# Optimization experiments

Hardware: AMD Instinct MI355X
Metric: run time of the kernel (lower is better)

Reference implementation:

```python
import jax, jax.numpy as jnp
import numpy as np

BETA = 0.1
IGNORE_INDEX = -100
B, T, H, V = 4, 512, 2048, 32000


def setup_inputs() -> dict:
    key = jax.random.key(0)
    k1, k2, k3, k4, k5 = jax.random.split(key, 5)
    x = jax.random.normal(k1, (B, T, H), dtype=jnp.float32)
    ref_x = jax.random.normal(k2, (B, T, H), dtype=jnp.float32)
    y = jax.random.randint(k3, (B, T), 0, V, dtype=jnp.int64)
    W = jax.random.normal(k4, (V, H), dtype=jnp.float32) * 0.02
    ref_W = jax.random.normal(k5, (V, H), dtype=jnp.float32) * 0.02
    return {"x": x, "ref_x": ref_x, "y": y, "W": W, "ref_W": ref_W}


def _avg_logps(inp, weight, target):
    # inp: [B,T,H], weight: [V,H], target: [B,T]
    logits = jnp.einsum('bth,vh->btv', inp, weight)          # [B,T,V]
    lse = jax.nn.logsumexp(logits, axis=-1)                  # [B,T]
    mask = (target != IGNORE_INDEX)
    safe = jnp.where(mask, target, 0)
    tok = jnp.take_along_axis(logits, safe[..., None], axis=-1)[..., 0]
    per_token_logps = tok - lse                               # [B,T]
    mask_f = mask.astype(per_token_logps.dtype)
    return (per_token_logps * mask_f).sum(-1) / mask_f.sum(-1)  # [B]


def reference(x, ref_x, y, W, ref_W):
    half = y.shape[0] // 2
    policy_logps = _avg_logps(x, W, y)
    # reference model runs under no_grad in the original
    ref_logps = jax.lax.stop_gradient(_avg_logps(ref_x, ref_W, y))
    logratios = policy_logps - ref_logps                      # [B]
    kl = jnp.zeros((), dtype=logratios.dtype)                 # kl=None -> 0
    chosen_losses = 1.0 - jax.nn.sigmoid(BETA * (logratios[:half] - kl))
    rejected_losses = 1.0 - jax.nn.sigmoid(BETA * (kl - logratios[half:]))
    return (chosen_losses.sum() + rejected_losses.sum()) / half
```

## Files before the change

kernel.cpp:

```cpp
#include <hip/hip_runtime.h>
#include <stdint.h>

#define B_DIM 4
#define T_DIM 512
#define NTOK  2048
#define H_DIM 2048
#define V_DIM 32000
#define BETA   0.1f
#define IGNORE_INDEX (-100)

#define TM    128
#define TN    128
#define BK    64
#define NCHUNK 250
#define NCH8  125
#define NTILE8 8

typedef _Float16 f16;
typedef _Float16 half8 __attribute__((ext_vector_type(8)));
typedef float    f32x4 __attribute__((ext_vector_type(4)));

#define AS1(p) ((const __attribute__((address_space(1))) unsigned int*)(p))
#define AS3(p) ((__attribute__((address_space(3))) unsigned int*)(p))

__global__ __launch_bounds__(256) void cvt_f32_f16(const float* __restrict__ src,
                                                   f16* __restrict__ dst, int n) {
    int i = (blockIdx.x * 256 + threadIdx.x) * 8;
    if (i + 8 > n) return;
    float4 v0 = *(const float4*)(src + i);
    float4 v1 = *(const float4*)(src + i + 4);
    half8 h = { (f16)v0.x, (f16)v0.y, (f16)v0.z, (f16)v0.w,
                (f16)v1.x, (f16)v1.y, (f16)v1.z, (f16)v1.w };
    *(half8*)(dst + i) = h;
}


#define DSR(d, a, IMM) \
    asm volatile("ds_read_b128 %0, %1 offset:%2" : "=v"(d) : "v"(a), "n"(IMM))

#define KTSTEP(BUF, KTW) do {                                                  \
    half8 af[4];                                                               \
    DSR(af[0], A_rd, (BUF) * 32768 + 0);                                       \
    DSR(af[1], A_rd, (BUF) * 32768 + 256);                                     \
    DSR(af[2], A_rd, (BUF) * 32768 + 512);                                     \
    DSR(af[3], A_rd, (BUF) * 32768 + 768);                                     \
    DSR(bfp[0], B_rd, (BUF) * 32768 + 0);                                      \
    DSR(bfp[1], B_rd, (BUF) * 32768 + 256);                                    \
    DSR(bfp[2], B_rd, (BUF) * 32768 + 512);                                    \
    DSR(bfp[3], B_rd, (BUF) * 32768 + 768);                                    \
    {                                                                          \
        const f16* sA = pA + (KTW) * 32;                                       \
        const f16* sB = pB + (KTW) * 32;                                       \
        f16* tA = dA + ((BUF) ^ 1) * 16384;                                    \
        f16* tB = dB + ((BUF) ^ 1) * 16384;                                    \
        __builtin_amdgcn_global_load_lds(AS1(sA),      AS3(tA),        16, 0, 0); \
        __builtin_amdgcn_global_load_lds(AS1(sA + 16), AS3(tA + 4096), 16, 0, 0); \
        __builtin_amdgcn_global_load_lds(AS1(sB),      AS3(tB),        16, 0, 0); \
        __builtin_amdgcn_global_load_lds(AS1(sB + 16), AS3(tB + 4096), 16, 0, 0); \
    }                                                                          \
    __builtin_amdgcn_s_barrier();                                              \
    asm volatile("s_waitcnt lgkmcnt(0)" ::: "memory");                         \
    __builtin_amdgcn_sched_barrier(0);                                         \
    __builtin_amdgcn_s_setprio(1);                                             \
    _Pragma("unroll")                                                          \
    for (int m_ = 0; m_ < 4; ++m_)                                             \
        _Pragma("unroll")                                                      \
        for (int n_ = 0; n_ < 4; ++n_)                                         \
            acc[m_][n_] = __builtin_amdgcn_mfma_f32_16x16x32_f16(              \
                af[m_], bfp[n_], acc[m_][n_], 0, 0, 0);                        \
    __builtin_amdgcn_s_setprio(0);                                             \
    __builtin_amdgcn_s_barrier();                                              \
    DSR(af[0], A_rd, (BUF) * 32768 + 1024 + 0);                                \
    DSR(af[1], A_rd, (BUF) * 32768 + 1024 + 256);                              \
    DSR(af[2], A_rd, (BUF) * 32768 + 1024 + 512);                              \
    DSR(af[3], A_rd, (BUF) * 32768 + 1024 + 768);                              \
    __builtin_amdgcn_s_barrier();                                              \
    asm volatile("s_waitcnt lgkmcnt(0)" ::: "memory");                         \
    __builtin_amdgcn_sched_barrier(0);                                         \
    __builtin_amdgcn_s_setprio(1);                                             \
    _Pragma("unroll")                                                          \
    for (int m_ = 0; m_ < 4; ++m_)                                             \
        _Pragma("unroll")                                                      \
        for (int n_ = 0; n_ < 4; ++n_)                                         \
            acc[4 + m_][n_] = __builtin_amdgcn_mfma_f32_16x16x32_f16(          \
                af[m_], bfp[n_], acc[4 + m_][n_], 0, 0, 0);                    \
    __builtin_amdgcn_s_setprio(0);                                             \
    asm volatile("s_waitcnt vmcnt(0)" ::: "memory");                           \
    __builtin_amdgcn_s_barrier();                                              \
} while (0)

__global__ __launch_bounds__(512, 2) void gemm_lse8(
    const f16* __restrict__ x0, const f16* __restrict__ x1,
    const f16* __restrict__ w0, const f16* __restrict__ w1,
    const int* __restrict__ y,
    float2* __restrict__ pMS,
    float* __restrict__ tokL)
{
    const int orig = blockIdx.x;
    const int wg   = (orig & 7) * 250 + (orig >> 3);
    const int tile = wg & 7;
    const int rest = wg >> 3;
    const int chunk = rest % NCH8;
    const int model = rest / NCH8;

    const f16* Xp = model ? x1 : x0;
    const f16* Wp = model ? w1 : w0;

    const int tid  = threadIdx.x;
    const int lane = tid & 63;
    const int wave = tid >> 6;
    const int wm   = wave >> 2;
    const int wn   = wave & 3;

    __shared__ __align__(16) f16 sm[2][2][4][256][8];
    __shared__ int ys[256];

    const int rowA0 = tile * 256;
    const int rowB0 = chunk * 256;

    f32x4 acc[8][4];
#pragma unroll
    for (int i = 0; i < 8; ++i)
#pragma unroll
        for (int j = 0; j < 4; ++j) acc[i][j] = (f32x4){0.f, 0.f, 0.f, 0.f};

    const int rS = tid & 255;
    const int cS = tid >> 8;
    const f16* pA = Xp + (size_t)(rowA0 + rS) * H_DIM + cS * 8;
    const f16* pB = Wp + (size_t)(rowB0 + rS) * H_DIM + cS * 8;
    f16* dA = &sm[0][0][0][0][0] + (size_t)tid * 8;
    f16* dB = dA + 8192;

    auto* smp3 = (__attribute__((address_space(3))) f16*)&sm[0][0][0][0][0];
    const unsigned smBase = (unsigned)(uintptr_t)smp3;
    const unsigned A_rd = smBase + ((unsigned)(lane >> 4) << 12)
                        + (((unsigned)(wm * 128 + (lane & 15))) << 4);
    const unsigned B_rd = smBase + 16384u + ((unsigned)(lane >> 4) << 12)
                        + (((unsigned)(wn * 64 + (lane & 15))) << 4);

    half8 bfp[4];

    int yreg = 0;
    if (tid < 256) yreg = y[rowA0 + tid];
    __builtin_amdgcn_global_load_lds(AS1(pA),      AS3(dA),        16, 0, 0);
    __builtin_amdgcn_global_load_lds(AS1(pA + 16), AS3(dA + 4096), 16, 0, 0);
    __builtin_amdgcn_global_load_lds(AS1(pB),      AS3(dB),        16, 0, 0);
    __builtin_amdgcn_global_load_lds(AS1(pB + 16), AS3(dB + 4096), 16, 0, 0);
    asm volatile("s_waitcnt vmcnt(0)" ::: "memory");
    if (tid < 256) ys[tid] = yreg;
    __builtin_amdgcn_s_barrier();

#pragma unroll 1
    for (int it = 0; it < 32; ++it) {
        KTSTEP(0, (2 * it + 1) & 63);
        KTSTEP(1, (2 * it + 2) & 63);
    }

    float* redM = (float*)&sm[0][0][0][0][0];
    float* redS = (float*)(&sm[0][0][0][0][0] + 2048);

#pragma unroll
    for (int i2 = 0; i2 < 8; ++i2) {
#pragma unroll
        for (int r = 0; r < 4; ++r) {
            int rl = wm * 128 + i2 * 16 + ((lane >> 4) << 2) + r;
            int t = ys[rl];
            int trel = t - (rowB0 + wn * 64);
#pragma unroll
            for (int j = 0; j < 4; ++j) {
                if (trel == j * 16 + (lane & 15))
                    tokL[model * NTOK + rowA0 + rl] = acc[i2][j][r];
            }
        }
    }

#pragma unroll
    for (int i2 = 0; i2 < 8; ++i2) {
#pragma unroll
        for (int r = 0; r < 4; ++r) {
            float mx = fmaxf(fmaxf(acc[i2][0][r], acc[i2][1][r]),
                             fmaxf(acc[i2][2][r], acc[i2][3][r]));
            for (int m = 1; m < 16; m <<= 1) mx = fmaxf(mx, __shfl_xor(mx, m, 64));
            float s = 0.f;
#pragma unroll
            for (int j = 0; j < 4; ++j) s += __expf(acc[i2][j][r] - mx);
            for (int m = 1; m < 16; m <<= 1) s += __shfl_xor(s, m, 64);
            if ((lane & 15) == 0) {
                int rl = wm * 128 + i2 * 16 + ((lane >> 4) << 2) + r;
                redM[rl * 4 + wn] = mx;
                redS[rl * 4 + wn] = s;
            }
        }
    }
    __syncthreads();
    if (tid < 256) {
        float M = redM[tid * 4 + 0], S = redS[tid * 4 + 0];
#pragma unroll
        for (int q = 1; q < 4; ++q) {
            float m2 = redM[tid * 4 + q], s2 = redS[tid * 4 + q];
            float Mn = fmaxf(M, m2);
            S = S * __expf(M - Mn) + s2 * __expf(m2 - Mn);
            M = Mn;
        }
        size_t o = ((size_t)model * NTOK + rowA0 + tid) * NCH8 + chunk;
        pMS[o] = make_float2(M, S);
    }
}

__global__ __launch_bounds__(256, 3) void gemm_lse_f32(
    const float* __restrict__ x0, const float* __restrict__ x1,
    const float* __restrict__ w0, const float* __restrict__ w1,
    const int* __restrict__ y,
    float2* __restrict__ pMS,
    float* __restrict__ tokL)
{
    const int tile  = blockIdx.x;
    const int chunk = blockIdx.y;
    const int model = blockIdx.z;
    const float* Xp = model ? x1 : x0;
    const float* Wp = model ? w1 : w0;

    const int tid  = threadIdx.x;
    const int lane = tid & 63;
    const int wave = tid >> 6;
    const int wm   = wave >> 1;
    const int wn   = wave & 1;

    __shared__ __align__(16) f16 As[8][TM][8];
    __shared__ __align__(16) f16 Bs[8][TN][8];
    __shared__ float redM[TM][2];
    __shared__ float redS[TM][2];
    __shared__ int   ys[TM];

    if (tid < TM) ys[tid] = y[tile * TM + tid];

    f32x4 acc[4][4];
#pragma unroll
    for (int i = 0; i < 4; ++i)
#pragma unroll
        for (int j = 0; j < 4; ++j) acc[i][j] = (f32x4){0.f, 0.f, 0.f, 0.f};

    const int rowA0 = tile * TM;
    const int rowB0 = chunk * TN;
    const int kc    = lane >> 4;
    const int rS = tid & 127;
    const int cS = tid >> 7;

    const float* pA = Xp + (size_t)(rowA0 + rS) * H_DIM + cS * 8;
    const float* pB = Wp + (size_t)(rowB0 + rS) * H_DIM + cS * 8;
    f16* dA = &As[0][0][0] + tid * 8;
    f16* dB = &Bs[0][0][0] + tid * 8;

    for (int k0 = 0; k0 < H_DIM; k0 += BK) {
#pragma unroll
        for (int i = 0; i < 4; ++i) {
            float4 v0 = *(const float4*)(pA + i * 16);
            float4 v1 = *(const float4*)(pA + i * 16 + 4);
            half8 h = { (f16)v0.x, (f16)v0.y, (f16)v0.z, (f16)v0.w,
                        (f16)v1.x, (f16)v1.y, (f16)v1.z, (f16)v1.w };
            *(half8*)(dA + i * 2048) = h;
        }
#pragma unroll
        for (int i = 0; i < 4; ++i) {
            float4 v0 = *(const float4*)(pB + i * 16);
            float4 v1 = *(const float4*)(pB + i * 16 + 4);
            half8 h = { (f16)v0.x, (f16)v0.y, (f16)v0.z, (f16)v0.w,
                        (f16)v1.x, (f16)v1.y, (f16)v1.z, (f16)v1.w };
            *(half8*)(dB + i * 2048) = h;
        }
        pA += BK; pB += BK;
        __syncthreads();

#pragma unroll
        for (int p = 0; p < 2; ++p) {
            half8 af[4], bfr[4];
#pragma unroll
            for (int i = 0; i < 4; ++i)
                af[i] = *(const half8*)As[p * 4 + kc][wm * 64 + i * 16 + (lane & 15)];
#pragma unroll
            for (int j = 0; j < 4; ++j)
                bfr[j] = *(const half8*)Bs[p * 4 + kc][wn * 64 + j * 16 + (lane & 15)];
#pragma unroll
            for (int i = 0; i < 4; ++i)
#pragma unroll
                for (int j = 0; j < 4; ++j)
                    acc[i][j] = __builtin_amdgcn_mfma_f32_16x16x32_f16(af[i], bfr[j], acc[i][j], 0, 0, 0);
        }
        __syncthreads();
    }

#pragma unroll
    for (int i = 0; i < 4; ++i) {
#pragma unroll
        for (int r = 0; r < 4; ++r) {
            int rl = wm * 64 + i * 16 + ((lane >> 4) << 2) + r;
            int t = ys[rl];
            int trel = t - (rowB0 + wn * 64);
#pragma unroll
            for (int j = 0; j < 4; ++j) {
                if (trel == j * 16 + (lane & 15))
                    tokL[model * NTOK + rowA0 + rl] = acc[i][j][r];
            }
        }
    }

#pragma unroll
    for (int i = 0; i < 4; ++i) {
#pragma unroll
        for (int r = 0; r < 4; ++r) {
            float mx = fmaxf(fmaxf(acc[i][0][r], acc[i][1][r]),
                             fmaxf(acc[i][2][r], acc[i][3][r]));
            for (int m = 1; m < 16; m <<= 1) mx = fmaxf(mx, __shfl_xor(mx, m, 64));
            float s = 0.f;
#pragma unroll
            for (int j = 0; j < 4; ++j) s += __expf(acc[i][j][r] - mx);
            for (int m = 1; m < 16; m <<= 1) s += __shfl_xor(s, m, 64);
            if ((lane & 15) == 0) {
                int rl = wm * 64 + i * 16 + ((lane >> 4) << 2) + r;
                redM[rl][wn] = mx;
                redS[rl][wn] = s;
            }
        }
    }
    __syncthreads();
    if (tid < TM) {
        float m0 = redM[tid][0], m1 = redM[tid][1];
        float s0 = redS[tid][0], s1 = redS[tid][1];
        float M = fmaxf(m0, m1);
        float S = s0 * __expf(m0 - M) + s1 * __expf(m1 - M);
        size_t o = ((size_t)model * NTOK + tile * TM + tid) * NCHUNK + chunk;
        pMS[o] = make_float2(M, S);
    }
}

__global__ __launch_bounds__(256) void lse_reduce(const float2* __restrict__ pMS,
                                                  const float* __restrict__ tokL,
                                                  const int* __restrict__ y,
                                                  float* __restrict__ logp,
                                                  int nchunk) {
    int g = blockIdx.x * 4 + (threadIdx.x >> 6);
    int lane = threadIdx.x & 63;
    const float2* base = pMS + (size_t)g * nchunk;
    float M = -1e30f, S = 0.f;
    for (int c = lane; c < nchunk; c += 64) {
        float2 ms = base[c];
        if (ms.x > M) { S = S * __expf(M - ms.x) + ms.y; M = ms.x; }
        else          { S += ms.y * __expf(ms.x - M); }
    }
#pragma unroll
    for (int off = 1; off < 64; off <<= 1) {
        float Mo = __shfl_xor(M, off, 64);
        float So = __shfl_xor(S, off, 64);
        float Mn = fmaxf(M, Mo);
        S = S * __expf(M - Mn) + So * __expf(Mo - Mn);
        M = Mn;
    }
    if (lane == 0) {
        float lse = M + logf(S);
        int token = g & (NTOK - 1);
        int t = y[token];
        logp[g] = (t == IGNORE_INDEX) ? 0.f : (tokL[g] - lse);
    }
}

__device__ __forceinline__ float sigf(float z) { return 1.f / (1.f + expf(-z)); }

__global__ void final_loss(const float* __restrict__ logp,
                           const int* __restrict__ y,
                           float* __restrict__ out) {
    int lane = threadIdx.x;
    float avg[2][4];
    for (int model = 0; model < 2; ++model)
        for (int b = 0; b < 4; ++b) {
            float s = 0.f, c = 0.f;
            for (int t = lane; t < T_DIM; t += 64) {
                int token = b * T_DIM + t;
                if (y[token] != IGNORE_INDEX) { s += logp[model * NTOK + token]; c += 1.f; }
            }
            for (int m = 1; m < 64; m <<= 1) {
                s += __shfl_xor(s, m, 64);
                c += __shfl_xor(c, m, 64);
            }
            avg[model][b] = s / c;
        }
    if (lane == 0) {
        float loss = 0.f;
        for (int b = 0; b < 2; ++b) {
            float lr = avg[0][b] - avg[1][b];
            loss += 1.f - sigf(BETA * lr);
        }
        for (int b = 2; b < 4; ++b) {
            float lr = avg[0][b] - avg[1][b];
            loss += 1.f - sigf(-BETA * lr);
        }
        out[0] = loss * 0.5f;
    }
}

extern "C" void kernel_launch(void* const* d_in, const int* in_sizes, int n_in,
                              void* d_out, int out_size, void* d_ws, size_t ws_size,
                              hipStream_t stream) {
    const float* x  = (const float*)d_in[0];
    const float* rx = (const float*)d_in[1];
    const int*   y  = (const int*)d_in[2];
    const float* W  = (const float*)d_in[3];
    const float* rW = (const float*)d_in[4];
    float* out = (float*)d_out;

    const size_t nX = (size_t)NTOK * H_DIM;
    const size_t nW = (size_t)V_DIM * H_DIM;

    char* p = (char*)d_ws;
    float2* pMS = (float2*)p; p += (size_t)2 * NTOK * NCHUNK * 8;
    float* tokL = (float*)p;  p += (size_t)2 * NTOK * 4;
    float* logp = (float*)p;  p += (size_t)2 * NTOK * 4;
    size_t base = (size_t)(p - (char*)d_ws);
    size_t need_fast = base + 2 * nX * 2 + 2 * nW * 2;

    if (ws_size >= need_fast) {
        f16* xb  = (f16*)p; p += nX * 2;
        f16* rxb = (f16*)p; p += nX * 2;
        f16* wb  = (f16*)p; p += nW * 2;
        f16* rwb = (f16*)p; p += nW * 2;
        cvt_f32_f16<<<(int)(nX / 8 / 256), 256, 0, stream>>>(x,  xb,  (int)nX);
        cvt_f32_f16<<<(int)(nX / 8 / 256), 256, 0, stream>>>(rx, rxb, (int)nX);
        cvt_f32_f16<<<(int)(nW / 8 / 256), 256, 0, stream>>>(W,  wb,  (int)nW);
        cvt_f32_f16<<<(int)(nW / 8 / 256), 256, 0, stream>>>(rW, rwb, (int)nW);
        gemm_lse8<<<dim3(NTILE8 * NCH8 * 2), 512, 0, stream>>>(xb, rxb, wb, rwb, y, pMS, tokL);
        lse_reduce<<<1024, 256, 0, stream>>>(pMS, tokL, y, logp, NCH8);
    } else {
        gemm_lse_f32<<<dim3(NTOK / TM, NCHUNK, 2), 256, 0, stream>>>(x, rx, W, rW, y, pMS, tokL);
        lse_reduce<<<1024, 256, 0, stream>>>(pMS, tokL, y, logp, NCHUNK);
    }
    final_loss<<<1, 64, 0, stream>>>(logp, y, out);
}
```

Before: 1.500 ms.

## Double K-depth per pipeline stage and simplify LDS reads and barriers

Each double-buffered stage now stages 64 K-elements instead of 32, which halves the number of main-loop iterations and barrier rounds. The hand-written inline-asm ds_read sequence with its split barriers and explicit waitcnts is replaced by plain C++ LDS loads, grouped into four sub-phases per stage with one __syncthreads at the end. The B fragments are reused across the two halves of the M tile. Shared memory doubles to about 128KB per block, which likely cuts residency to one 512-thread block per CU and weakens latency hiding.

```diff
diff --git a/kernel.cpp b/kernel.cpp
--- a/kernel.cpp
+++ b/kernel.cpp
@@ -34,60 +34,6 @@
     *(half8*)(dst + i) = h;
 }
 
-
-#define DSR(d, a, IMM) \
-    asm volatile("ds_read_b128 %0, %1 offset:%2" : "=v"(d) : "v"(a), "n"(IMM))
-
-#define KTSTEP(BUF, KTW) do {                                                  \
-    half8 af[4];                                                               \
-    DSR(af[0], A_rd, (BUF) * 32768 + 0);                                       \
-    DSR(af[1], A_rd, (BUF) * 32768 + 256);                                     \
-    DSR(af[2], A_rd, (BUF) * 32768 + 512);                                     \
-    DSR(af[3], A_rd, (BUF) * 32768 + 768);                                     \
-    DSR(bfp[0], B_rd, (BUF) * 32768 + 0);                                      \
-    DSR(bfp[1], B_rd, (BUF) * 32768 + 256);                                    \
-    DSR(bfp[2], B_rd, (BUF) * 32768 + 512);                                    \
-    DSR(bfp[3], B_rd, (BUF) * 32768 + 768);                                    \
-    {                                                                          \
-        const f16* sA = pA + (KTW) * 32;                                       \
-        const f16* sB = pB + (KTW) * 32;                                       \
-        f16* tA = dA + ((BUF) ^ 1) * 16384;                                    \
-        f16* tB = dB + ((BUF) ^ 1) * 16384;                                    \
-        __builtin_amdgcn_global_load_lds(AS1(sA),      AS3(tA),        16, 0, 0); \
-        __builtin_amdgcn_global_load_lds(AS1(sA + 16), AS3(tA + 4096), 16, 0, 0); \
-        __builtin_amdgcn_global_load_lds(AS1(sB),      AS3(tB),        16, 0, 0); \
-        __builtin_amdgcn_global_load_lds(AS1(sB + 16), AS3(tB + 4096), 16, 0, 0); \
-    }                                                                          \
-    __builtin_amdgcn_s_barrier();                                              \
-    asm volatile("s_waitcnt lgkmcnt(0)" ::: "memory");                         \
-    __builtin_amdgcn_sched_barrier(0);                                         \
-    __builtin_amdgcn_s_setprio(1);                                             \
-    _Pragma("unroll")                                                          \
-    for (int m_ = 0; m_ < 4; ++m_)                                             \
-        _Pragma("unroll")                                                      \
-        for (int n_ = 0; n_ < 4; ++n_)                                         \
-            acc[m_][n_] = __builtin_amdgcn_mfma_f32_16x16x32_f16(              \
-                af[m_], bfp[n_], acc[m_][n_], 0, 0, 0);                        \
-    __builtin_amdgcn_s_setprio(0);                                             \
-    __builtin_amdgcn_s_barrier();                                              \
-    DSR(af[0], A_rd, (BUF) * 32768 + 1024 + 0);                                \
-    DSR(af[1], A_rd, (BUF) * 32768 + 1024 + 256);                              \
-    DSR(af[2], A_rd, (BUF) * 32768 + 1024 + 512);                              \
-    DSR(af[3], A_rd, (BUF) * 32768 + 1024 + 768);                              \
-    __builtin_amdgcn_s_barrier();                                              \
-    asm volatile("s_waitcnt lgkmcnt(0)" ::: "memory");                         \
-    __builtin_amdgcn_sched_barrier(0);                                         \
-    __builtin_amdgcn_s_setprio(1);                                             \
-    _Pragma("unroll")                                                          \
-    for (int m_ = 0; m_ < 4; ++m_)                                             \
-        _Pragma("unroll")                                                      \
-        for (int n_ = 0; n_ < 4; ++n_)                                         \
-            acc[4 + m_][n_] = __builtin_amdgcn_mfma_f32_16x16x32_f16(          \
-                af[m_], bfp[n_], acc[4 + m_][n_], 0, 0, 0);                    \
-    __builtin_amdgcn_s_setprio(0);                                             \
-    asm volatile("s_waitcnt vmcnt(0)" ::: "memory");                           \
-    __builtin_amdgcn_s_barrier();                                              \
-} while (0)
 
 __global__ __launch_bounds__(512, 2) void gemm_lse8(
     const f16* __restrict__ x0, const f16* __restrict__ x1,
@@ -111,8 +57,10 @@
     const int wave = tid >> 6;
     const int wm   = wave >> 2;
     const int wn   = wave & 3;
-
-    __shared__ __align__(16) f16 sm[2][2][4][256][8];
+    const int ln   = lane & 15;
+    const int kq   = lane >> 4;
+
+    __shared__ __align__(16) f16 sm[2][2][8][256][8];
     __shared__ int ys[256];
 
     const int rowA0 = tile * 256;
@@ -129,31 +77,60 @@
     const f16* pA = Xp + (size_t)(rowA0 + rS) * H_DIM + cS * 8;
     const f16* pB = Wp + (size_t)(rowB0 + rS) * H_DIM + cS * 8;
     f16* dA = &sm[0][0][0][0][0] + (size_t)tid * 8;
-    f16* dB = dA + 8192;
-
-    auto* smp3 = (__attribute__((address_space(3))) f16*)&sm[0][0][0][0][0];
-    const unsigned smBase = (unsigned)(uintptr_t)smp3;
-    const unsigned A_rd = smBase + ((unsigned)(lane >> 4) << 12)
-                        + (((unsigned)(wm * 128 + (lane & 15))) << 4);
-    const unsigned B_rd = smBase + 16384u + ((unsigned)(lane >> 4) << 12)
-                        + (((unsigned)(wn * 64 + (lane & 15))) << 4);
+    f16* dB = dA + 16384;
+
+#define STAGE8(NB, KT) do {                                                    \
+    const int kw_ = (KT) & 31;                                                 \
+    const f16* sa_ = pA + kw_ * 64;                                            \
+    const f16* sb_ = pB + kw_ * 64;                                            \
+    f16* ta_ = dA + (NB) * 32768;                                              \
+    f16* tb_ = dB + (NB) * 32768;                                              \
+    _Pragma("unroll")                                                          \
+    for (int i_ = 0; i_ < 4; ++i_) {                                           \
+        __builtin_amdgcn_global_load_lds(AS1(sa_ + i_ * 16), AS3(ta_ + i_ * 4096), 16, 0, 0); \
+        __builtin_amdgcn_global_load_lds(AS1(sb_ + i_ * 16), AS3(tb_ + i_ * 4096), 16, 0, 0); \
+    }                                                                          \
+} while (0)
+
+#define SUBPHASE(B, P, FH) do {                                                \
+    half8 af[4];                                                               \
+    if ((FH) == 0) {                                                           \
+        _Pragma("unroll")                                                      \
+        for (int j_ = 0; j_ < 4; ++j_)                                         \
+            bfp[j_] = *(const half8*)&sm[B][1][(P) * 4 + kq][wn * 64 + j_ * 16 + ln][0]; \
+    }                                                                          \
+    _Pragma("unroll")                                                          \
+    for (int i_ = 0; i_ < 4; ++i_)                                             \
+        af[i_] = *(const half8*)&sm[B][0][(P) * 4 + kq][wm * 128 + (FH) * 64 + i_ * 16 + ln][0]; \
+    __builtin_amdgcn_s_setprio(1);                                             \
+    _Pragma("unroll")                                                          \
+    for (int i_ = 0; i_ < 4; ++i_)                                             \
+        _Pragma("unroll")                                                      \
+        for (int j_ = 0; j_ < 4; ++j_)                                         \
+            acc[(FH) * 4 + i_][j_] = __builtin_amdgcn_mfma_f32_16x16x32_f16(   \
+                af[i_], bfp[j_], acc[(FH) * 4 + i_][j_], 0, 0, 0);             \
+    __builtin_amdgcn_s_setprio(0);                                             \
+} while (0)
+
+#define KTSTEP(B, KTN) do {                                                    \
+    STAGE8((B) ^ 1, KTN);                                                      \
+    SUBPHASE(B, 0, 0);                                                         \
+    SUBPHASE(B, 0, 1);                                                         \
+    SUBPHASE(B, 1, 0);                                                         \
+    SUBPHASE(B, 1, 1);                                                         \
+    __syncthreads();                                                           \
+} while (0)
 
     half8 bfp[4];
 
-    int yreg = 0;
-    if (tid < 256) yreg = y[rowA0 + tid];
-    __builtin_amdgcn_global_load_lds(AS1(pA),      AS3(dA),        16, 0, 0);
-    __builtin_amdgcn_global_load_lds(AS1(pA + 16), AS3(dA + 4096), 16, 0, 0);
-    __builtin_amdgcn_global_load_lds(AS1(pB),      AS3(dB),        16, 0, 0);
-    __builtin_amdgcn_global_load_lds(AS1(pB + 16), AS3(dB + 4096), 16, 0, 0);
-    asm volatile("s_waitcnt vmcnt(0)" ::: "memory");
-    if (tid < 256) ys[tid] = yreg;
-    __builtin_amdgcn_s_barrier();
+    if (tid < 256) ys[tid] = y[rowA0 + tid];
+    STAGE8(0, 0);
+    __syncthreads();
 
 #pragma unroll 1
-    for (int it = 0; it < 32; ++it) {
-        KTSTEP(0, (2 * it + 1) & 63);
-        KTSTEP(1, (2 * it + 2) & 63);
+    for (int it = 0; it < 16; ++it) {
+        KTSTEP(0, 2 * it + 1);
+        KTSTEP(1, 2 * it + 2);
     }
 
     float* redM = (float*)&sm[0][0][0][0][0];
@@ -163,12 +140,12 @@
     for (int i2 = 0; i2 < 8; ++i2) {
 #pragma unroll
         for (int r = 0; r < 4; ++r) {
-            int rl = wm * 128 + i2 * 16 + ((lane >> 4) << 2) + r;
+            int rl = wm * 128 + i2 * 16 + (kq << 2) + r;
             int t = ys[rl];
             int trel = t - (rowB0 + wn * 64);
 #pragma unroll
             for (int j = 0; j < 4; ++j) {
-                if (trel == j * 16 + (lane & 15))
+                if (trel == j * 16 + ln)
                     tokL[model * NTOK + rowA0 + rl] = acc[i2][j][r];
             }
         }
@@ -185,8 +162,8 @@
 #pragma unroll
             for (int j = 0; j < 4; ++j) s += __expf(acc[i2][j][r] - mx);
             for (int m = 1; m < 16; m <<= 1) s += __shfl_xor(s, m, 64);
-            if ((lane & 15) == 0) {
-                int rl = wm * 128 + i2 * 16 + ((lane >> 4) << 2) + r;
+            if (ln == 0) {
+                int rl = wm * 128 + i2 * 16 + (kq << 2) + r;
                 redM[rl * 4 + wn] = mx;
                 redS[rl * 4 + wn] = s;
             }
@@ -205,6 +182,9 @@
         size_t o = ((size_t)model * NTOK + rowA0 + tid) * NCH8 + chunk;
         pMS[o] = make_float2(M, S);
     }
+#undef STAGE8
+#undef SUBPHASE
+#undef KTSTEP
 }
 
 __global__ __launch_bounds__(256, 3) void gemm_lse_f32(
```

New measurement: 1.783 ms. 18.8% more time.
